# Kernel tuning notes

Hardware: AMD Instinct MI355X
Metric: run time of the kernel (lower is better)

## Reference

```python
import jax, jax.numpy as jnp
import numpy as np

NL = 192
SCALE = 1.5
SH_C0 = 0.28209479177387814
SH_C1 = 0.4886025119029199
SH_C2 = [1.0925484305920792, -1.0925484305920792, 0.31539156525252005, -1.0925484305920792, 0.5462742152960396]


def sh_eval(k, d):
    # k: (N, 3, 9) SH coeffs, d: (N, 3) directions -> (N, 3) rgb
    x, y, z = d[..., 0:1], d[..., 1:2], d[..., 2:3]
    return (SH_C0 * k[..., 0]
            - SH_C1 * y * k[..., 1]
            + SH_C1 * z * k[..., 2]
            - SH_C1 * x * k[..., 3]
            + SH_C2[0] * x * y * k[..., 4]
            + SH_C2[1] * y * z * k[..., 5]
            + SH_C2[2] * (2.0 * z * z - x * x - y * y) * k[..., 6]
            + SH_C2[3] * x * z * k[..., 7]
            + SH_C2[4] * (x * x - y * y) * k[..., 8])


def setup_inputs() -> dict:
    key = jax.random.key(0)
    k1, k2 = jax.random.split(key)
    N = 1048576
    x = jax.random.normal(k1, (N, 3), dtype=jnp.float32)
    d = jax.random.normal(k2, (N, 3), dtype=jnp.float32)
    voxel = jnp.ones((NL, NL, NL, 28), dtype=jnp.float32) / 100.0
    return {"x": x, "d": d, "voxel": voxel}


def reference(x, d, voxel):
    xs = x / SCALE
    mask = jnp.all(jnp.abs(xs) < 0.5, axis=1)  # (N,)
    # continuous grid coordinates, clipped like the original
    idx = jnp.clip(xs / (2.0 / NL) + NL / 2.0, 0.0, NL - 1.0)  # (N,3)
    xf = jnp.floor(idx)
    xc = jnp.ceil(idx)
    f = xf.astype(jnp.int32)
    c = xc.astype(jnp.int32)
    # 8 vertices in the ORIGINAL module's ordering (incl. its patch-layout quirk)
    vx = jnp.stack([f[:, 0], c[:, 0], f[:, 0], f[:, 0], f[:, 0], c[:, 0], c[:, 0], c[:, 0]], axis=1)
    vy = jnp.stack([f[:, 1], f[:, 1], c[:, 1], f[:, 1], c[:, 1], f[:, 1], c[:, 1], c[:, 1]], axis=1)
    vz = jnp.stack([f[:, 2], f[:, 2], f[:, 2], c[:, 2], c[:, 2], c[:, 2], f[:, 2], c[:, 2]], axis=1)
    v = voxel[vx, vy, vz]  # (N, 8, 28) gather
    # grid_sample trilinear weights on the 2x2x2 patch: slot j=(dd,hh,ww),
    # w-frac = t0, h-frac = t1, d-frac = t2 (align_corners=False, size 2 => frac = t)
    t = idx - xf  # (N,3)
    t0, t1, t2 = t[:, 0], t[:, 1], t[:, 2]
    u0, u1, u2 = 1.0 - t0, 1.0 - t1, 1.0 - t2
    w = jnp.stack([u2 * u1 * u0, u2 * u1 * t0, u2 * t1 * u0, u2 * t1 * t0,
                   t2 * u1 * u0, t2 * u1 * t0, t2 * t1 * u0, t2 * t1 * t0], axis=1)  # (N,8)
    feat = jnp.einsum('nk,nkc->nc', w, v)  # (N,28)
    sigma = jnp.where(mask, jax.nn.relu(feat[:, 0]), 0.0)  # (N,)
    k = feat[:, 1:].reshape(-1, 3, 9)
    color = jnp.where(mask[:, None], sh_eval(k, d), 0.0)  # (N,3)
    return color, sigma
```

## Files before the change

kernel.cpp:

```cpp
#include <hip/hip_runtime.h>


#define VNL 192
#define BLK 256
#define WPB 4
#define TILES 4
#define PTS (BLK * TILES)

#define SH_C0f 0.28209479177387814f
#define SH_C1f 0.4886025119029199f
#define C2_0f  1.0925484305920792f
#define C2_1f (-1.0925484305920792f)
#define C2_2f  0.31539156525252005f
#define C2_3f (-1.0925484305920792f)
#define C2_4f  0.5462742152960396f

template <int CTRL>
__device__ __forceinline__ float dpp_add(float v) {
    int s = __builtin_amdgcn_update_dpp(0, __float_as_int(v), CTRL, 0xF, 0xF, true);
    return v + __int_as_float(s);
}

__global__ __launch_bounds__(BLK) void plen_fused_kernel(
    const float* __restrict__ x,
    const float* __restrict__ d,
    const float* __restrict__ voxel,
    float* __restrict__ out,
    int N)
{
    __shared__ __align__(16) float4 s_pool[PTS][2];
    __shared__ __align__(16) float  s_xbuf[3 * PTS];
    __shared__ unsigned s_wcnt[TILES][WPB];

    const int tid  = threadIdx.x;
    const int wid  = tid >> 6;
    const int lane = tid & 63;
    const int g = lane >> 3;
    const int j = lane & 7;
    const int base_i = blockIdx.x * PTS;
    const int rem = N - base_i;
    const bool full = (rem >= PTS);

    const float4 z4 = make_float4(0.f, 0.f, 0.f, 0.f);

    if (full && (((3 * base_i) & 3) == 0)) {
        float4* cf4 = reinterpret_cast<float4*>(out) + ((3 * base_i) >> 2);
        #pragma unroll
        for (int k = 0; k < 3; ++k) cf4[k * BLK + tid] = z4;
    } else {
        for (int k = tid; k < 3 * (rem < PTS ? rem : PTS); k += BLK)
            out[3 * base_i + k] = 0.f;
    }
    if (full && (((3 * N + base_i) & 3) == 0)) {
        float4* sf4 = reinterpret_cast<float4*>(out + (size_t)3 * N + base_i);
        sf4[tid] = z4;
    } else {
        for (int k = tid; k < (rem < PTS ? rem : PTS); k += BLK)
            out[(size_t)3 * N + base_i + k] = 0.f;
    }

    if (full && (((3 * base_i) & 3) == 0)) {
        const float4* xf4 = reinterpret_cast<const float4*>(x) + ((3 * base_i) >> 2);
        float4* sb4 = reinterpret_cast<float4*>(s_xbuf);
        #pragma unroll
        for (int k = 0; k < 3; ++k) sb4[k * BLK + tid] = xf4[k * BLK + tid];
    } else {
        for (int k = tid; k < 3 * (rem < PTS ? rem : PTS); k += BLK)
            s_xbuf[k] = x[3 * base_i + k];
    }
    __syncthreads();

    unsigned Mrun = 0;
    for (int t = 0; t < TILES; ++t) {
        int p = t * BLK + tid;
        int i = base_i + p;
        bool act = false;
        float ix = 0.f, iy = 0.f, iz = 0.f;
        float vdx = 0.f, vdy = 0.f, vdz = 0.f;
        if (i < N) {
            float px = s_xbuf[3 * p + 0] / 1.5f;
            float py = s_xbuf[3 * p + 1] / 1.5f;
            float pz = s_xbuf[3 * p + 2] / 1.5f;
            act = (fabsf(px) < 0.5f) && (fabsf(py) < 0.5f) && (fabsf(pz) < 0.5f);
            if (act) {
                const float step = 2.0f / (float)VNL;
                ix = fminf(fmaxf(px / step + (float)(VNL / 2), 0.0f), (float)(VNL - 1));
                iy = fminf(fmaxf(py / step + (float)(VNL / 2), 0.0f), (float)(VNL - 1));
                iz = fminf(fmaxf(pz / step + (float)(VNL / 2), 0.0f), (float)(VNL - 1));
                vdx = d[3 * i + 0];
                vdy = d[3 * i + 1];
                vdz = d[3 * i + 2];
            }
        }

        unsigned long long bal = __ballot(act);
        unsigned wtot = (unsigned)__popcll(bal);
        unsigned pre  = (unsigned)__popcll(bal & ((1ull << lane) - 1ull));
        if (lane == 0) s_wcnt[t][wid] = wtot;
        __syncthreads();

        unsigned n0 = s_wcnt[t][0], n1 = s_wcnt[t][1];
        unsigned n2 = s_wcnt[t][2], n3 = s_wcnt[t][3];
        unsigned wbase = Mrun + (wid > 0 ? n0 : 0u) + (wid > 1 ? n1 : 0u)
                              + (wid > 2 ? n2 : 0u);
        if (act) {
            unsigned slot = wbase + pre;
            s_pool[slot][0] = make_float4(ix, iy, iz, __int_as_float(i));
            s_pool[slot][1] = make_float4(vdx, vdy, vdz, 0.f);
        }
        Mrun += n0 + n1 + n2 + n3;
    }
    __syncthreads();

    const unsigned M = Mrun;
    if (M == 0) return;
    const unsigned nch = (M + 7u) >> 3;

    for (unsigned c = (unsigned)wid; c < nch; c += WPB) {
        unsigned r = c * 8u + (unsigned)g;
        bool on = (r < M);
        unsigned rr = on ? r : (M - 1u);

        float4 e0 = s_pool[rr][0];
        float4 e1 = s_pool[rr][1];

        float fx = floorf(e0.x), fy = floorf(e0.y), fz = floorf(e0.z);
        int f0 = (int)fx, f1 = (int)fy, f2 = (int)fz;
        int c0i = (int)ceilf(e0.x), c1i = (int)ceilf(e0.y), c2i = (int)ceilf(e0.z);
        float t0 = e0.x - fx, t1 = e0.y - fy, t2 = e0.z - fz;

        float wj = ((j & 4) ? t2 : 1.0f - t2) * ((j & 2) ? t1 : 1.0f - t1)
                 * ((j & 1) ? t0 : 1.0f - t0);

        int X = ((0xE2 >> j) & 1) ? c0i : f0;
        int Y = ((0xD4 >> j) & 1) ? c1i : f1;
        int Z = ((0xB8 >> j) & 1) ? c2i : f2;
        const char* cell = (const char*)voxel
            + (size_t)(unsigned)(((X * VNL + Y) * VNL + Z) * 112);

        float4 v0 = *(const float4*)(cell +  0);
        float4 v1 = *(const float4*)(cell + 16);
        float4 v2 = *(const float4*)(cell + 32);
        float4 v3 = *(const float4*)(cell + 48);
        float4 v4 = *(const float4*)(cell + 64);
        float4 v5 = *(const float4*)(cell + 80);
        float4 v6 = *(const float4*)(cell + 96);

        float pdx = e1.x, pdy = e1.y, pdz = e1.z;
        float b1c = -SH_C1f * pdy;
        float b2c =  SH_C1f * pdz;
        float b3c = -SH_C1f * pdx;
        float b4c = C2_0f * pdx * pdy;
        float b5c = C2_1f * pdy * pdz;
        float b6c = C2_2f * (2.0f * pdz * pdz - pdx * pdx - pdy * pdy);
        float b7c = C2_3f * pdx * pdz;
        float b8c = C2_4f * (pdx * pdx - pdy * pdy);

        float cc0 = SH_C0f*v0.y + b1c*v0.z + b2c*v0.w + b3c*v1.x + b4c*v1.y
                  + b5c*v1.z + b6c*v1.w + b7c*v2.x + b8c*v2.y;
        float cc1 = SH_C0f*v2.z + b1c*v2.w + b2c*v3.x + b3c*v3.y + b4c*v3.z
                  + b5c*v3.w + b6c*v4.x + b7c*v4.y + b8c*v4.z;
        float cc2 = SH_C0f*v4.w + b1c*v5.x + b2c*v5.y + b3c*v5.z + b4c*v5.w
                  + b5c*v6.x + b6c*v6.y + b7c*v6.z + b8c*v6.w;
        cc0 *= wj; cc1 *= wj; cc2 *= wj;
        float ff0 = wj * v0.x;

        cc0 = dpp_add<0xB1>(cc0);  cc1 = dpp_add<0xB1>(cc1);
        cc2 = dpp_add<0xB1>(cc2);  ff0 = dpp_add<0xB1>(ff0);
        cc0 = dpp_add<0x4E>(cc0);  cc1 = dpp_add<0x4E>(cc1);
        cc2 = dpp_add<0x4E>(cc2);  ff0 = dpp_add<0x4E>(ff0);
        cc0 = dpp_add<0x141>(cc0); cc1 = dpp_add<0x141>(cc1);
        cc2 = dpp_add<0x141>(cc2); ff0 = dpp_add<0x141>(ff0);

        if (on && j < 4) {
            int pi = __float_as_int(e0.w);
            float rv = (j == 0) ? cc0 : (j == 1) ? cc1 : (j == 2) ? cc2
                                                      : fmaxf(ff0, 0.0f);
            size_t a = (j < 3) ? ((size_t)3 * pi + j) : ((size_t)3 * N + pi);
            out[a] = rv;
        }
    }
}

extern "C" void kernel_launch(void* const* d_in, const int* in_sizes, int n_in,
                              void* d_out, int out_size, void* d_ws, size_t ws_size,
                              hipStream_t stream) {
    const float* x     = (const float*)d_in[0];
    const float* d     = (const float*)d_in[1];
    const float* voxel = (const float*)d_in[2];
    float* out = (float*)d_out;
    int N = in_sizes[0] / 3;

    int grid = (N + PTS - 1) / PTS;
    plen_fused_kernel<<<grid, BLK, 0, stream>>>(x, d, voxel, out, N);
}
```

Before: 47.89 us.

## Split each voxel cell load across four lanes per vertex, two points per wave

The gather phase changes from 8 lanes per point (one lane per vertex, each loading all 7 float4s) to 32 lanes per point: 8 vertices times 4 lanes, each lane loading at most two float4s of the 112-byte cell. Each lane computes a partial SH dot product for its channel slice. The partials are reduced with DPP adds plus cross-lane shuffles over offsets 4, 8 and 16. The goal is fewer registers and less per-lane load latency, with more lanes active in flight. The cost is that each wave now covers only 2 points instead of 8, so the loop runs more iterations and the shuffle reduction gets longer.

New measurement: 60.70 us. 1.27x slower.

```diff
diff --git a/kernel.cpp b/kernel.cpp
--- a/kernel.cpp
+++ b/kernel.cpp
@@ -35,8 +35,6 @@
     const int tid  = threadIdx.x;
     const int wid  = tid >> 6;
     const int lane = tid & 63;
-    const int g = lane >> 3;
-    const int j = lane & 7;
     const int base_i = blockIdx.x * PTS;
     const int rem = N - base_i;
     const bool full = (rem >= PTS);
@@ -114,69 +112,87 @@
 
     const unsigned M = Mrun;
     if (M == 0) return;
-    const unsigned nch = (M + 7u) >> 3;
-
-    for (unsigned c = (unsigned)wid; c < nch; c += WPB) {
-        unsigned r = c * 8u + (unsigned)g;
-        bool on = (r < M);
-        unsigned rr = on ? r : (M - 1u);
-
-        float4 e0 = s_pool[rr][0];
-        float4 e1 = s_pool[rr][1];
+    const unsigned npair = (M + 1u) >> 1;
+
+    const int jj = (lane >> 2) & 7;
+    const int q  = lane & 3;
+
+    for (unsigned pr = (unsigned)wid; pr < npair; pr += WPB) {
+        unsigned p = 2u * pr + (unsigned)(lane >> 5);
+        bool on = (p < M);
+        unsigned pc = on ? p : (M - 1u);
+
+        float4 e0 = s_pool[pc][0];
+        float4 e1 = s_pool[pc][1];
 
         float fx = floorf(e0.x), fy = floorf(e0.y), fz = floorf(e0.z);
-        int f0 = (int)fx, f1 = (int)fy, f2 = (int)fz;
+        int f0i = (int)fx, f1i = (int)fy, f2i = (int)fz;
         int c0i = (int)ceilf(e0.x), c1i = (int)ceilf(e0.y), c2i = (int)ceilf(e0.z);
         float t0 = e0.x - fx, t1 = e0.y - fy, t2 = e0.z - fz;
 
-        float wj = ((j & 4) ? t2 : 1.0f - t2) * ((j & 2) ? t1 : 1.0f - t1)
-                 * ((j & 1) ? t0 : 1.0f - t0);
-
-        int X = ((0xE2 >> j) & 1) ? c0i : f0;
-        int Y = ((0xD4 >> j) & 1) ? c1i : f1;
-        int Z = ((0xB8 >> j) & 1) ? c2i : f2;
+        float wj = ((jj & 4) ? t2 : 1.0f - t2) * ((jj & 2) ? t1 : 1.0f - t1)
+                 * ((jj & 1) ? t0 : 1.0f - t0);
+        int X = ((0xE2 >> jj) & 1) ? c0i : f0i;
+        int Y = ((0xD4 >> jj) & 1) ? c1i : f1i;
+        int Z = ((0xB8 >> jj) & 1) ? c2i : f2i;
         const char* cell = (const char*)voxel
             + (size_t)(unsigned)(((X * VNL + Y) * VNL + Z) * 112);
 
-        float4 v0 = *(const float4*)(cell +  0);
-        float4 v1 = *(const float4*)(cell + 16);
-        float4 v2 = *(const float4*)(cell + 32);
-        float4 v3 = *(const float4*)(cell + 48);
-        float4 v4 = *(const float4*)(cell + 64);
-        float4 v5 = *(const float4*)(cell + 80);
-        float4 v6 = *(const float4*)(cell + 96);
+        float4 va = *(const float4*)(cell + 16 * q);
+        float4 vb = z4;
+        if (q < 3) vb = *(const float4*)(cell + 64 + 16 * q);
 
         float pdx = e1.x, pdy = e1.y, pdz = e1.z;
-        float b1c = -SH_C1f * pdy;
-        float b2c =  SH_C1f * pdz;
-        float b3c = -SH_C1f * pdx;
-        float b4c = C2_0f * pdx * pdy;
-        float b5c = C2_1f * pdy * pdz;
-        float b6c = C2_2f * (2.0f * pdz * pdz - pdx * pdx - pdy * pdy);
-        float b7c = C2_3f * pdx * pdz;
-        float b8c = C2_4f * (pdx * pdx - pdy * pdy);
-
-        float cc0 = SH_C0f*v0.y + b1c*v0.z + b2c*v0.w + b3c*v1.x + b4c*v1.y
-                  + b5c*v1.z + b6c*v1.w + b7c*v2.x + b8c*v2.y;
-        float cc1 = SH_C0f*v2.z + b1c*v2.w + b2c*v3.x + b3c*v3.y + b4c*v3.z
-                  + b5c*v3.w + b6c*v4.x + b7c*v4.y + b8c*v4.z;
-        float cc2 = SH_C0f*v4.w + b1c*v5.x + b2c*v5.y + b3c*v5.z + b4c*v5.w
-                  + b5c*v6.x + b6c*v6.y + b7c*v6.z + b8c*v6.w;
-        cc0 *= wj; cc1 *= wj; cc2 *= wj;
-        float ff0 = wj * v0.x;
-
-        cc0 = dpp_add<0xB1>(cc0);  cc1 = dpp_add<0xB1>(cc1);
-        cc2 = dpp_add<0xB1>(cc2);  ff0 = dpp_add<0xB1>(ff0);
-        cc0 = dpp_add<0x4E>(cc0);  cc1 = dpp_add<0x4E>(cc1);
-        cc2 = dpp_add<0x4E>(cc2);  ff0 = dpp_add<0x4E>(ff0);
-        cc0 = dpp_add<0x141>(cc0); cc1 = dpp_add<0x141>(cc1);
-        cc2 = dpp_add<0x141>(cc2); ff0 = dpp_add<0x141>(ff0);
-
-        if (on && j < 4) {
+        float b1 = -SH_C1f * pdy;
+        float b2 =  SH_C1f * pdz;
+        float b3 = -SH_C1f * pdx;
+        float b4 = C2_0f * pdx * pdy;
+        float b5 = C2_1f * pdy * pdz;
+        float b6 = C2_2f * (2.0f * pdz * pdz - pdx * pdx - pdy * pdy);
+        float b7 = C2_3f * pdx * pdz;
+        float b8 = C2_4f * (pdx * pdx - pdy * pdy);
+
+        float f0a = 0.f, cc0 = 0.f, cc1 = 0.f, cc2 = 0.f;
+        switch (q) {
+        case 0:
+            f0a = va.x;
+            cc0 = SH_C0f * va.y + b1 * va.z + b2 * va.w;
+            cc1 = b6 * vb.x + b7 * vb.y + b8 * vb.z;
+            cc2 = SH_C0f * vb.w;
+            break;
+        case 1:
+            cc0 = b3 * va.x + b4 * va.y + b5 * va.z + b6 * va.w;
+            cc2 = b1 * vb.x + b2 * vb.y + b3 * vb.z + b4 * vb.w;
+            break;
+        case 2:
+            cc0 = b7 * va.x + b8 * va.y;
+            cc1 = SH_C0f * va.z + b1 * va.w;
+            cc2 = b5 * vb.x + b6 * vb.y + b7 * vb.z + b8 * vb.w;
+            break;
+        default:
+            cc1 = b2 * va.x + b3 * va.y + b4 * va.z + b5 * va.w;
+            break;
+        }
+        f0a *= wj; cc0 *= wj; cc1 *= wj; cc2 *= wj;
+
+        f0a = dpp_add<0xB1>(f0a); cc0 = dpp_add<0xB1>(cc0);
+        cc1 = dpp_add<0xB1>(cc1); cc2 = dpp_add<0xB1>(cc2);
+        f0a = dpp_add<0x4E>(f0a); cc0 = dpp_add<0x4E>(cc0);
+        cc1 = dpp_add<0x4E>(cc1); cc2 = dpp_add<0x4E>(cc2);
+        #pragma unroll
+        for (int m = 4; m <= 16; m <<= 1) {
+            f0a += __shfl_xor(f0a, m);
+            cc0 += __shfl_xor(cc0, m);
+            cc1 += __shfl_xor(cc1, m);
+            cc2 += __shfl_xor(cc2, m);
+        }
+
+        int sub = lane & 31;
+        if (on && sub < 4) {
             int pi = __float_as_int(e0.w);
-            float rv = (j == 0) ? cc0 : (j == 1) ? cc1 : (j == 2) ? cc2
-                                                      : fmaxf(ff0, 0.0f);
-            size_t a = (j < 3) ? ((size_t)3 * pi + j) : ((size_t)3 * N + pi);
+            float rv = (sub == 0) ? cc0 : (sub == 1) ? cc1 : (sub == 2) ? cc2
+                                                          : fmaxf(f0a, 0.0f);
+            size_t a = (sub < 3) ? ((size_t)3 * pi + sub) : ((size_t)3 * N + pi);
             out[a] = rv;
         }
     }
```
